# Kernel optimization log

Measured on AMD Instinct MI355X. Metric: run time of the kernel, lower is better.

The kernel has to match this reference:

```python
import jax, jax.numpy as jnp
import numpy as np

NUM_HEADS = 2
LN_EPS = 1e-5
NEG_MASK = -1e9


def setup_inputs() -> dict:
    key = jax.random.key(0)
    ks = jax.random.split(key, 8)
    B, C, T, N = 8, 64, 32, 400
    H, D = NUM_HEADS, C // NUM_HEADS
    s = 1.0 / np.sqrt(C)
    return {
        "x": jax.random.normal(ks[0], (B, C, T, N), dtype=jnp.float32),
        "Wq": jax.random.normal(ks[1], (C, C), dtype=jnp.float32) * s,
        "Wk": jax.random.normal(ks[2], (C, C), dtype=jnp.float32) * s,
        "Wv": jax.random.normal(ks[3], (C, C), dtype=jnp.float32) * s,
        "a_src": jax.random.normal(ks[4], (H, D), dtype=jnp.float32) * 0.1,
        "a_dst": jax.random.normal(ks[5], (H, D), dtype=jnp.float32) * 0.1,
        "ln_gamma": jnp.ones((C,), dtype=jnp.float32),
        "ln_beta": jnp.zeros((C,), dtype=jnp.float32),
        "gso": jax.random.randint(ks[6], (N, N), 0, 2, dtype=jnp.int32),
    }


def reference(x, Wq, Wk, Wv, a_src, a_dst, ln_gamma, ln_beta, gso):
    B, C, T, N = x.shape
    H = NUM_HEADS
    D = C // H
    # (B,C,T,N) -> (B*T, N, C)
    xr = jnp.transpose(x, (0, 2, 3, 1)).reshape(B * T, N, C)
    # torch Linear: y = x @ W.T; then split heads -> (BT, N, H, D)
    Q = (xr @ Wq.T).reshape(B * T, N, H, D)
    K = (xr @ Wk.T).reshape(B * T, N, H, D)
    V = (xr @ Wv.T).reshape(B * T, N, H, D)
    # GAT additive scores per head
    s_src = jnp.einsum("bnhd,hd->bnh", Q, a_src)  # (BT, N, H)
    s_dst = jnp.einsum("bnhd,hd->bnh", K, a_dst)  # (BT, N, H)
    scores = s_src[:, :, None, :] + s_dst[:, None, :, :]  # (BT, i, j, H)
    scores = jax.nn.leaky_relu(scores, negative_slope=0.2)
    mask = jnp.where(gso == 0, jnp.float32(NEG_MASK), 0.0)  # (N, N)
    scores = scores + mask[None, :, :, None]
    attn = jax.nn.softmax(scores, axis=2)  # softmax over dst j; dropout = identity (eval)
    out = jnp.einsum("bijh,bjhd->bihd", attn, V).reshape(B * T, N, C)
    # LayerNorm over channel dim
    mu = jnp.mean(out, axis=-1, keepdims=True)
    var = jnp.var(out, axis=-1, keepdims=True)
    out = (out - mu) * jax.lax.rsqrt(var + LN_EPS) * ln_gamma + ln_beta
    # (BT, N, C) -> (B, C, T, N)
    return jnp.transpose(out.reshape(B, T, N, C), (0, 3, 1, 2))
```

## Files before the change

### kernel.cpp

```cpp
#include <hip/hip_runtime.h>
#include <hip/hip_bf16.h>

typedef __attribute__((ext_vector_type(8))) short bf16x8;
typedef __attribute__((ext_vector_type(4))) float f32x4;
typedef __attribute__((ext_vector_type(4))) int i32x4;
typedef __attribute__((ext_vector_type(4))) unsigned int u32x4;

#define B_   8
#define C_   64
#define T_   32
#define N_   400
#define BT_  256
#define NKT_ 13
#define CN_  12800
#define VROW 424
#define WROW 72
#define L2E_ 1.4426950408889634f
#define C2_  (-13.849872392533959f)
#define SH12_ (-17.312340490667560f)

#if __has_builtin(__builtin_amdgcn_exp2f)
#define EXP2F(x) __builtin_amdgcn_exp2f(x)
#else
#define EXP2F(x) __expf((x) * 0.6931471805599453f)
#endif

__global__ __launch_bounds__(256) void gat_prep(
    const int* __restrict__ gso, unsigned int* __restrict__ mb)
{
  int idx = blockIdx.x*256 + threadIdx.x;
  if (idx < N_*16) {
    int i = idx >> 4, kw = idx & 15;
    unsigned int bits = 0;
    if (kw < 13) {
      int j0 = kw * 32;
      #pragma unroll
      for (int bb = 0; bb < 32; ++bb) {
        int j = j0 + bb;
        if (j < N_ && gso[i*N_ + j] != 0) bits |= (1u << bb);
      }
    }
    mb[idx] = bits;
  }
}

__global__ __launch_bounds__(1024) void gat_fused(
    const float* __restrict__ x, const float* __restrict__ Wq,
    const float* __restrict__ Wk, const float* __restrict__ Wv,
    const float* __restrict__ a_src, const float* __restrict__ a_dst,
    const float* __restrict__ gamma, const float* __restrict__ beta,
    const unsigned int* __restrict__ mb, float* __restrict__ out)
{
  __shared__ __align__(16) __hip_bfloat16 Vt[64][VROW];
  __shared__ __align__(16) __hip_bfloat16 wvb[80][WROW];
  __shared__ __align__(16) float sd_s[2][416];
  __shared__ __align__(16) float si_s[2][400];
  __shared__ __align__(16) float ob[128][68];
  __shared__ float g_s[64], b_s[64];

  const int tid = threadIdx.x;
  const int bt = blockIdx.x;
  const int b = bt >> 5, t = bt & 31;
  const int lane = tid & 63, wave = tid >> 6;
  const int col = lane & 15, quad = lane >> 4;

  #pragma unroll
  for (int it = 0; it < 4; ++it) {
    int idx = it*1024 + tid;
    int o = idx >> 6, c = idx & 63;
    wvb[o][c] = __float2bfloat16(Wv[o*C_ + c]);
  }
  if (tid < 256) {
    int ww = tid >> 6, c = tid & 63, h = ww >> 1;
    const float* W = (ww & 1) ? Wk : Wq;
    const float* a = (ww & 1) ? a_dst : a_src;
    float s = 0.f;
    #pragma unroll
    for (int d = 0; d < 32; ++d) s += W[(h*32 + d)*C_ + c] * a[h*32 + d];
    wvb[64 + ww][c] = __float2bfloat16(s * L2E_);
  } else if (tid < 320) {
    g_s[tid - 256] = gamma[tid - 256];
  } else if (tid < 384) {
    b_s[tid - 320] = beta[tid - 320];
  } else if (tid < 416) {
    int tt = tid - 384;
    sd_s[tt >> 4][400 + (tt & 15)] = 0.f;
  }
  for (int idx = tid; idx < 12*WROW; idx += 1024)
    wvb[68 + idx/WROW][idx % WROW] = __float2bfloat16(0.f);
  for (int idx = tid; idx < 64*24; idx += 1024)
    Vt[idx/24][400 + idx%24] = __float2bfloat16(0.f);
  __syncthreads();

  {
    const float* xbase = x + ((size_t)b*C_*T_ + t)*N_;
    for (int nt = wave; nt < 25; nt += 16) {
      const int n0 = nt*16;
      bf16x8 bfrag[2];
      #pragma unroll
      for (int kt = 0; kt < 2; ++kt) {
        const float* xc = xbase + (size_t)(kt*32 + quad*8)*CN_ + n0 + col;
        union { short s[8]; bf16x8 v; } pk;
        #pragma unroll
        for (int j = 0; j < 8; ++j) {
          union { __hip_bfloat16 h; short s; } cv;
          cv.h = __float2bfloat16(xc[(size_t)j*CN_]);
          pk.s[j] = cv.s;
        }
        bfrag[kt] = pk.v;
      }
      #pragma unroll
      for (int ot = 0; ot < 5; ++ot) {
        f32x4 acc = {0.f, 0.f, 0.f, 0.f};
        #pragma unroll
        for (int kt = 0; kt < 2; ++kt) {
          bf16x8 afr = *(const bf16x8*)&wvb[ot*16 + col][kt*32 + quad*8];
          acc = __builtin_amdgcn_mfma_f32_16x16x32_bf16(afr, bfrag[kt], acc, 0, 0, 0);
        }
        if (ot < 4) {
          #pragma unroll
          for (int r = 0; r < 4; ++r)
            Vt[ot*16 + quad*4 + r][n0 + col] = __float2bfloat16(acc[r]);
        } else if (quad == 0) {
          #pragma unroll
          for (int r = 0; r < 4; ++r) {
            int h = r >> 1;
            if (r & 1) sd_s[h][n0 + col] = acc[r];
            else       si_s[h][n0 + col] = acc[r] + SH12_;
          }
        }
      }
    }
  }
  __syncthreads();

  const int hh = wave & 1, itile = wave >> 1;
  const int rowA = col;

  bf16x8 ones;
  #pragma unroll
  for (int k = 0; k < 8; ++k) ones[k] = (short)0x3F80;

  for (int r0 = 0; r0 < N_; r0 += 128) {
    const int ibase = r0 + itile*16;
    if (ibase < N_) {
      const int irow = ibase + rowA;
      const float si1 = si_s[hh][irow];
      const u32x4* mp = (const u32x4*)(mb + irow*16);
      u32x4 mw0 = mp[0], mw1 = mp[1], mw2 = mp[2];
      unsigned int mw12 = mb[irow*16 + 12];
      const float* sdp = sd_s[hh] + quad*8;
      const __hip_bfloat16* v0p = &Vt[hh*32 + rowA][quad*8];
      const __hip_bfloat16* v1p = v0p + 16*VROW;

      f32x4 d0 = {0,0,0,0}, d1 = {0,0,0,0}, d2 = {0,0,0,0};
      #pragma unroll
      for (int kt = 0; kt < NKT_; ++kt) {
        unsigned int mword = (kt < 4) ? mw0[kt] : (kt < 8) ? mw1[kt-4]
                           : (kt < 12) ? mw2[kt-8] : mw12;
        unsigned int mbyte = (mword >> (quad*8)) & 0xffu;
        f32x4 s0 = *(const f32x4*)(sdp + kt*32);
        f32x4 s1 = *(const f32x4*)(sdp + kt*32 + 4);
        bf16x8 vb0 = *(const bf16x8*)(v0p + kt*32);
        bf16x8 vb1 = *(const bf16x8*)(v1p + kt*32);
        int em[8];
        #pragma unroll
        for (int jj = 0; jj < 8; ++jj) {
          float sd = (jj < 4) ? s0[jj] : s1[jj-4];
          float t1 = si1 + sd;
          float t2 = fmaf(0.2f, t1, C2_);
          float v  = fmaxf(t1, t2);
          float e  = EXP2F(v);
          int msk = ((int)(mbyte << (31 - jj))) >> 31;
          em[jj] = __float_as_int(e) & msk;
        }
        union { i32x4 i; bf16x8 v; } af;
        af.i.x = (int)__builtin_amdgcn_perm((unsigned)em[1], (unsigned)em[0], 0x07060302u);
        af.i.y = (int)__builtin_amdgcn_perm((unsigned)em[3], (unsigned)em[2], 0x07060302u);
        af.i.z = (int)__builtin_amdgcn_perm((unsigned)em[5], (unsigned)em[4], 0x07060302u);
        af.i.w = (int)__builtin_amdgcn_perm((unsigned)em[7], (unsigned)em[6], 0x07060302u);
        d0 = __builtin_amdgcn_mfma_f32_16x16x32_bf16(af.v, vb0, d0, 0, 0, 0);
        d1 = __builtin_amdgcn_mfma_f32_16x16x32_bf16(af.v, vb1, d1, 0, 0, 0);
        d2 = __builtin_amdgcn_mfma_f32_16x16x32_bf16(af.v, ones, d2, 0, 0, 0);
      }
      #pragma unroll
      for (int r = 0; r < 4; ++r) {
        float li = 1.0f / d2[r];
        int rl = itile*16 + quad*4 + r;
        ob[rl][hh*32 + rowA]      = d0[r] * li;
        ob[rl][hh*32 + 16 + rowA] = d1[r] * li;
      }
    }
    __syncthreads();

    {
      int rl = tid >> 3, cgi = tid & 7;
      int n = r0 + rl;
      if (n < N_) {
        float u[8]; float s = 0.f;
        #pragma unroll
        for (int k = 0; k < 8; ++k) { u[k] = ob[rl][cgi*8 + k]; s += u[k]; }
        s += __shfl_xor(s,1); s += __shfl_xor(s,2); s += __shfl_xor(s,4);
        float mu = s * (1.f/64.f);
        float q = 0.f;
        #pragma unroll
        for (int k = 0; k < 8; ++k) { float dv = u[k]-mu; q = fmaf(dv,dv,q); }
        q += __shfl_xor(q,1); q += __shfl_xor(q,2); q += __shfl_xor(q,4);
        float rstd = rsqrtf(q*(1.f/64.f) + 1e-5f);
        #pragma unroll
        for (int k = 0; k < 8; ++k)
          ob[rl][cgi*8 + k] = (u[k]-mu)*rstd*g_s[cgi*8 + k] + b_s[cgi*8 + k];
      }
    }
    __syncthreads();

    #pragma unroll
    for (int it = 0; it < 8; ++it) {
      int idx = it*1024 + tid;
      int c = idx >> 7, nn = idx & 127;
      int n = r0 + nn;
      if (n < N_) out[((size_t)(b*C_ + c)*T_ + t)*N_ + n] = ob[nn][c];
    }
    __syncthreads();
  }
}

extern "C" void kernel_launch(void* const* d_in, const int* in_sizes, int n_in,
                              void* d_out, int out_size, void* d_ws, size_t ws_size,
                              hipStream_t stream) {
  (void)in_sizes; (void)n_in; (void)out_size; (void)ws_size;
  const float* x     = (const float*)d_in[0];
  const float* Wq    = (const float*)d_in[1];
  const float* Wk    = (const float*)d_in[2];
  const float* Wv    = (const float*)d_in[3];
  const float* a_src = (const float*)d_in[4];
  const float* a_dst = (const float*)d_in[5];
  const float* gamma = (const float*)d_in[6];
  const float* beta  = (const float*)d_in[7];
  const int*   gso   = (const int*)d_in[8];
  float* out = (float*)d_out;

  unsigned int* mb = (unsigned int*)d_ws;

  gat_prep<<<26, 256, 0, stream>>>(gso, mb);
  gat_fused<<<BT_, 1024, 0, stream>>>(x, Wq, Wk, Wv, a_src, a_dst,
                                      gamma, beta, mb, out);
}
```

Before: 122.4 us.

## Split each batch-time slice across two 512-thread blocks with aliased LDS

Launches two 512-thread blocks per (b,t) slice, each handling half of the query rows, so there are 512 blocks instead of 256 with smaller per-block LDS. The wvb and ob buffers are aliased into one scratch array to cut shared memory. x loads for the projection are software-prefetched into registers one tile ahead. The cost is that each block recomputes the full V/score projection, doubling that work and the x reads.

```diff
diff --git a/kernel.cpp b/kernel.cpp
--- a/kernel.cpp
+++ b/kernel.cpp
@@ -15,6 +15,7 @@
 #define CN_  12800
 #define VROW 424
 #define WROW 72
+#define OBW  65
 #define L2E_ 1.4426950408889634f
 #define C2_  (-13.849872392533959f)
 #define SH12_ (-17.312340490667560f)
@@ -44,7 +45,7 @@
   }
 }
 
-__global__ __launch_bounds__(1024) void gat_fused(
+__global__ __launch_bounds__(512, 4) void gat_fused(
     const float* __restrict__ x, const float* __restrict__ Wq,
     const float* __restrict__ Wk, const float* __restrict__ Wv,
     const float* __restrict__ a_src, const float* __restrict__ a_dst,
@@ -52,21 +53,38 @@
     const unsigned int* __restrict__ mb, float* __restrict__ out)
 {
   __shared__ __align__(16) __hip_bfloat16 Vt[64][VROW];
-  __shared__ __align__(16) __hip_bfloat16 wvb[80][WROW];
+  __shared__ __align__(16) char scr[16640];
   __shared__ __align__(16) float sd_s[2][416];
   __shared__ __align__(16) float si_s[2][400];
-  __shared__ __align__(16) float ob[128][68];
   __shared__ float g_s[64], b_s[64];
 
+  __hip_bfloat16 (*wvb)[WROW] = (__hip_bfloat16(*)[WROW])scr;
+  float (*ob)[OBW] = (float(*)[OBW])scr;
+
   const int tid = threadIdx.x;
-  const int bt = blockIdx.x;
+  const int bt = blockIdx.x >> 1, half = blockIdx.x & 1;
   const int b = bt >> 5, t = bt & 31;
   const int lane = tid & 63, wave = tid >> 6;
   const int col = lane & 15, quad = lane >> 4;
+  const int i_start = half ? 208 : 0;
+  const int i_end   = half ? 400 : 208;
+
+  const float* xbase = x + ((size_t)b*C_*T_ + t)*N_;
+
+  float xf[16];
+  {
+    const int n0 = wave*16;
+    const float* xc0 = xbase + (size_t)(quad*8)*CN_ + n0 + col;
+    const float* xc1 = xbase + (size_t)(32 + quad*8)*CN_ + n0 + col;
+    #pragma unroll
+    for (int j = 0; j < 8; ++j) xf[j]     = xc0[(size_t)j*CN_];
+    #pragma unroll
+    for (int j = 0; j < 8; ++j) xf[8 + j] = xc1[(size_t)j*CN_];
+  }
 
   #pragma unroll
-  for (int it = 0; it < 4; ++it) {
-    int idx = it*1024 + tid;
+  for (int it = 0; it < 8; ++it) {
+    int idx = it*512 + tid;
     int o = idx >> 6, c = idx & 63;
     wvb[o][c] = __float2bfloat16(Wv[o*C_ + c]);
   }
@@ -86,48 +104,53 @@
     int tt = tid - 384;
     sd_s[tt >> 4][400 + (tt & 15)] = 0.f;
   }
-  for (int idx = tid; idx < 12*WROW; idx += 1024)
+  for (int idx = tid; idx < 12*WROW; idx += 512)
     wvb[68 + idx/WROW][idx % WROW] = __float2bfloat16(0.f);
-  for (int idx = tid; idx < 64*24; idx += 1024)
+  for (int idx = tid; idx < 64*24; idx += 512)
     Vt[idx/24][400 + idx%24] = __float2bfloat16(0.f);
   __syncthreads();
 
-  {
-    const float* xbase = x + ((size_t)b*C_*T_ + t)*N_;
-    for (int nt = wave; nt < 25; nt += 16) {
-      const int n0 = nt*16;
-      bf16x8 bfrag[2];
+  for (int nt = wave; nt < 25; nt += 8) {
+    const int n0 = nt*16;
+    bf16x8 bfrag[2];
+    #pragma unroll
+    for (int kt = 0; kt < 2; ++kt) {
+      union { short s[8]; bf16x8 v; } pk;
+      #pragma unroll
+      for (int j = 0; j < 8; ++j) {
+        union { __hip_bfloat16 h; short s; } cv;
+        cv.h = __float2bfloat16(xf[kt*8 + j]);
+        pk.s[j] = cv.s;
+      }
+      bfrag[kt] = pk.v;
+    }
+    const int ntn = nt + 8;
+    if (ntn < 25) {
+      const float* xc0 = xbase + (size_t)(quad*8)*CN_ + ntn*16 + col;
+      const float* xc1 = xbase + (size_t)(32 + quad*8)*CN_ + ntn*16 + col;
+      #pragma unroll
+      for (int j = 0; j < 8; ++j) xf[j]     = xc0[(size_t)j*CN_];
+      #pragma unroll
+      for (int j = 0; j < 8; ++j) xf[8 + j] = xc1[(size_t)j*CN_];
+    }
+    #pragma unroll
+    for (int ot = 0; ot < 5; ++ot) {
+      f32x4 acc = {0.f, 0.f, 0.f, 0.f};
       #pragma unroll
       for (int kt = 0; kt < 2; ++kt) {
-        const float* xc = xbase + (size_t)(kt*32 + quad*8)*CN_ + n0 + col;
-        union { short s[8]; bf16x8 v; } pk;
-        #pragma unroll
-        for (int j = 0; j < 8; ++j) {
-          union { __hip_bfloat16 h; short s; } cv;
-          cv.h = __float2bfloat16(xc[(size_t)j*CN_]);
-          pk.s[j] = cv.s;
-        }
-        bfrag[kt] = pk.v;
-      }
-      #pragma unroll
-      for (int ot = 0; ot < 5; ++ot) {
-        f32x4 acc = {0.f, 0.f, 0.f, 0.f};
-        #pragma unroll
-        for (int kt = 0; kt < 2; ++kt) {
-          bf16x8 afr = *(const bf16x8*)&wvb[ot*16 + col][kt*32 + quad*8];
-          acc = __builtin_amdgcn_mfma_f32_16x16x32_bf16(afr, bfrag[kt], acc, 0, 0, 0);
-        }
-        if (ot < 4) {
-          #pragma unroll
-          for (int r = 0; r < 4; ++r)
-            Vt[ot*16 + quad*4 + r][n0 + col] = __float2bfloat16(acc[r]);
-        } else if (quad == 0) {
-          #pragma unroll
-          for (int r = 0; r < 4; ++r) {
-            int h = r >> 1;
-            if (r & 1) sd_s[h][n0 + col] = acc[r];
-            else       si_s[h][n0 + col] = acc[r] + SH12_;
-          }
+        bf16x8 afr = *(const bf16x8*)&wvb[ot*16 + col][kt*32 + quad*8];
+        acc = __builtin_amdgcn_mfma_f32_16x16x32_bf16(afr, bfrag[kt], acc, 0, 0, 0);
+      }
+      if (ot < 4) {
+        #pragma unroll
+        for (int r = 0; r < 4; ++r)
+          Vt[ot*16 + quad*4 + r][n0 + col] = __float2bfloat16(acc[r]);
+      } else if (quad == 0) {
+        #pragma unroll
+        for (int r = 0; r < 4; ++r) {
+          int h = r >> 1;
+          if (r & 1) sd_s[h][n0 + col] = acc[r];
+          else       si_s[h][n0 + col] = acc[r] + SH12_;
         }
       }
     }
@@ -141,9 +164,9 @@
   #pragma unroll
   for (int k = 0; k < 8; ++k) ones[k] = (short)0x3F80;
 
-  for (int r0 = 0; r0 < N_; r0 += 128) {
+  for (int r0 = i_start; r0 < i_end; r0 += 64) {
     const int ibase = r0 + itile*16;
-    if (ibase < N_) {
+    if (ibase < i_end) {
       const int irow = ibase + rowA;
       const float si1 = si_s[hh][irow];
       const u32x4* mp = (const u32x4*)(mb + irow*16);
@@ -196,7 +219,7 @@
     {
       int rl = tid >> 3, cgi = tid & 7;
       int n = r0 + rl;
-      if (n < N_) {
+      if (n < i_end) {
         float u[8]; float s = 0.f;
         #pragma unroll
         for (int k = 0; k < 8; ++k) { u[k] = ob[rl][cgi*8 + k]; s += u[k]; }
@@ -216,10 +239,10 @@
 
     #pragma unroll
     for (int it = 0; it < 8; ++it) {
-      int idx = it*1024 + tid;
-      int c = idx >> 7, nn = idx & 127;
+      int idx = it*512 + tid;
+      int c = idx >> 6, nn = idx & 63;
       int n = r0 + nn;
-      if (n < N_) out[((size_t)(b*C_ + c)*T_ + t)*N_ + n] = ob[nn][c];
+      if (n < i_end) out[((size_t)(b*C_ + c)*T_ + t)*N_ + n] = ob[nn][c];
     }
     __syncthreads();
   }
@@ -243,6 +266,6 @@
   unsigned int* mb = (unsigned int*)d_ws;
 
   gat_prep<<<26, 256, 0, stream>>>(gso, mb);
-  gat_fused<<<BT_, 1024, 0, stream>>>(x, Wq, Wk, Wv, a_src, a_dst,
-                                      gamma, beta, mb, out);
+  gat_fused<<<BT_*2, 512, 0, stream>>>(x, Wq, Wk, Wv, a_src, a_dst,
+                                       gamma, beta, mb, out);
 }
```

New measurement: 126.7 us. +3.5%, slower.

## Fuse LayerNorm into attention waves and store output directly from registers

Applied to the files above, without the earlier changes.

Each wave now handles one 16-row tile for both heads and runs LayerNorm in registers using cross-lane shuffles. It then writes float4 vectors straight to global memory, which removes the shared ob buffer, the per-128-row passes and their three barriers. The x loads are issued before the weight setup so their latency overlaps it, the projection weight fragments are hoisted into registers, and the reciprocal uses the hardware rcp builtin. In exchange, waves are imbalanced (25 tiles over 16 waves), register pressure is higher, and rcp gives slightly lower precision.

```diff
diff --git a/kernel.cpp b/kernel.cpp
--- a/kernel.cpp
+++ b/kernel.cpp
@@ -24,6 +24,11 @@
 #else
 #define EXP2F(x) __expf((x) * 0.6931471805599453f)
 #endif
+#if __has_builtin(__builtin_amdgcn_rcpf)
+#define RCPF(x) __builtin_amdgcn_rcpf(x)
+#else
+#define RCPF(x) (1.0f / (x))
+#endif
 
 __global__ __launch_bounds__(256) void gat_prep(
     const int* __restrict__ gso, unsigned int* __restrict__ mb)
@@ -55,7 +60,6 @@
   __shared__ __align__(16) __hip_bfloat16 wvb[80][WROW];
   __shared__ __align__(16) float sd_s[2][416];
   __shared__ __align__(16) float si_s[2][400];
-  __shared__ __align__(16) float ob[128][68];
   __shared__ float g_s[64], b_s[64];
 
   const int tid = threadIdx.x;
@@ -63,6 +67,19 @@
   const int b = bt >> 5, t = bt & 31;
   const int lane = tid & 63, wave = tid >> 6;
   const int col = lane & 15, quad = lane >> 4;
+
+  const float* xbase = x + ((size_t)b*C_*T_ + t)*N_;
+
+  float xf[16];
+  {
+    const int n0 = wave*16;
+    const float* xc0 = xbase + (size_t)(quad*8)*CN_ + n0 + col;
+    const float* xc1 = xbase + (size_t)(32 + quad*8)*CN_ + n0 + col;
+    #pragma unroll
+    for (int j = 0; j < 8; ++j) xf[j]     = xc0[(size_t)j*CN_];
+    #pragma unroll
+    for (int j = 0; j < 8; ++j) xf[8 + j] = xc1[(size_t)j*CN_];
+  }
 
   #pragma unroll
   for (int it = 0; it < 4; ++it) {
@@ -86,47 +103,65 @@
     int tt = tid - 384;
     sd_s[tt >> 4][400 + (tt & 15)] = 0.f;
   }
-  for (int idx = tid; idx < 12*WROW; idx += 1024)
-    wvb[68 + idx/WROW][idx % WROW] = __float2bfloat16(0.f);
+  if (tid < 12*WROW)
+    wvb[68 + tid/WROW][tid % WROW] = __float2bfloat16(0.f);
   for (int idx = tid; idx < 64*24; idx += 1024)
     Vt[idx/24][400 + idx%24] = __float2bfloat16(0.f);
   __syncthreads();
 
   {
-    const float* xbase = x + ((size_t)b*C_*T_ + t)*N_;
-    for (int nt = wave; nt < 25; nt += 16) {
-      const int n0 = nt*16;
-      bf16x8 bfrag[2];
-      #pragma unroll
-      for (int kt = 0; kt < 2; ++kt) {
-        const float* xc = xbase + (size_t)(kt*32 + quad*8)*CN_ + n0 + col;
-        union { short s[8]; bf16x8 v; } pk;
-        #pragma unroll
-        for (int j = 0; j < 8; ++j) {
-          union { __hip_bfloat16 h; short s; } cv;
-          cv.h = __float2bfloat16(xc[(size_t)j*CN_]);
-          pk.s[j] = cv.s;
-        }
-        bfrag[kt] = pk.v;
-      }
-      #pragma unroll
-      for (int ot = 0; ot < 5; ++ot) {
-        f32x4 acc = {0.f, 0.f, 0.f, 0.f};
+    bf16x8 afr[5][2];
+    #pragma unroll
+    for (int ot = 0; ot < 5; ++ot)
+      #pragma unroll
+      for (int kt = 0; kt < 2; ++kt)
+        afr[ot][kt] = *(const bf16x8*)&wvb[ot*16 + col][kt*32 + quad*8];
+
+    const int nt2 = wave + 16;
+    float xg[16];
+    if (nt2 < 25) {
+      const float* xc0 = xbase + (size_t)(quad*8)*CN_ + nt2*16 + col;
+      const float* xc1 = xbase + (size_t)(32 + quad*8)*CN_ + nt2*16 + col;
+      #pragma unroll
+      for (int j = 0; j < 8; ++j) xg[j]     = xc0[(size_t)j*CN_];
+      #pragma unroll
+      for (int j = 0; j < 8; ++j) xg[8 + j] = xc1[(size_t)j*CN_];
+    }
+
+    #pragma unroll
+    for (int task = 0; task < 2; ++task) {
+      const int nt = (task == 0) ? wave : nt2;
+      if (nt < 25) {
+        const int n0 = nt*16;
+        const float* src = (task == 0) ? xf : xg;
+        bf16x8 bfrag[2];
         #pragma unroll
         for (int kt = 0; kt < 2; ++kt) {
-          bf16x8 afr = *(const bf16x8*)&wvb[ot*16 + col][kt*32 + quad*8];
-          acc = __builtin_amdgcn_mfma_f32_16x16x32_bf16(afr, bfrag[kt], acc, 0, 0, 0);
+          union { short s[8]; bf16x8 v; } pk;
+          #pragma unroll
+          for (int j = 0; j < 8; ++j) {
+            union { __hip_bfloat16 h; short s; } cv;
+            cv.h = __float2bfloat16(src[kt*8 + j]);
+            pk.s[j] = cv.s;
+          }
+          bfrag[kt] = pk.v;
         }
-        if (ot < 4) {
-          #pragma unroll
-          for (int r = 0; r < 4; ++r)
-            Vt[ot*16 + quad*4 + r][n0 + col] = __float2bfloat16(acc[r]);
-        } else if (quad == 0) {
-          #pragma unroll
-          for (int r = 0; r < 4; ++r) {
-            int h = r >> 1;
-            if (r & 1) sd_s[h][n0 + col] = acc[r];
-            else       si_s[h][n0 + col] = acc[r] + SH12_;
+        #pragma unroll
+        for (int ot = 0; ot < 5; ++ot) {
+          f32x4 acc = {0.f, 0.f, 0.f, 0.f};
+          acc = __builtin_amdgcn_mfma_f32_16x16x32_bf16(afr[ot][0], bfrag[0], acc, 0, 0, 0);
+          acc = __builtin_amdgcn_mfma_f32_16x16x32_bf16(afr[ot][1], bfrag[1], acc, 0, 0, 0);
+          if (ot < 4) {
+            #pragma unroll
+            for (int r = 0; r < 4; ++r)
+              Vt[ot*16 + quad*4 + r][n0 + col] = __float2bfloat16(acc[r]);
+          } else if (quad == 0) {
+            #pragma unroll
+            for (int r = 0; r < 4; ++r) {
+              int h = r >> 1;
+              if (r & 1) sd_s[h][n0 + col] = acc[r];
+              else       si_s[h][n0 + col] = acc[r] + SH12_;
+            }
           }
         }
       }
@@ -134,26 +169,29 @@
   }
   __syncthreads();
 
-  const int hh = wave & 1, itile = wave >> 1;
-  const int rowA = col;
-
-  bf16x8 ones;
+  float gg[4], bb[4];
   #pragma unroll
-  for (int k = 0; k < 8; ++k) ones[k] = (short)0x3F80;
-
-  for (int r0 = 0; r0 < N_; r0 += 128) {
-    const int ibase = r0 + itile*16;
-    if (ibase < N_) {
-      const int irow = ibase + rowA;
+  for (int k = 0; k < 4; ++k) { gg[k] = g_s[16*k + col]; bb[k] = b_s[16*k + col]; }
+
+  for (int tl = wave; tl < 25; tl += 16) {
+    const int ibase = tl*16;
+    const int irow = ibase + col;
+    const u32x4* mp = (const u32x4*)(mb + irow*16);
+    u32x4 mw0 = mp[0], mw1 = mp[1], mw2 = mp[2];
+    unsigned int mw12 = mb[irow*16 + 12];
+
+    float u[4][4];
+    #pragma unroll
+    for (int hh = 0; hh < 2; ++hh) {
       const float si1 = si_s[hh][irow];
-      const u32x4* mp = (const u32x4*)(mb + irow*16);
-      u32x4 mw0 = mp[0], mw1 = mp[1], mw2 = mp[2];
-      unsigned int mw12 = mb[irow*16 + 12];
       const float* sdp = sd_s[hh] + quad*8;
-      const __hip_bfloat16* v0p = &Vt[hh*32 + rowA][quad*8];
+      const __hip_bfloat16* v0p = &Vt[hh*32 + col][quad*8];
       const __hip_bfloat16* v1p = v0p + 16*VROW;
-
       f32x4 d0 = {0,0,0,0}, d1 = {0,0,0,0}, d2 = {0,0,0,0};
+      bf16x8 ones;
+      #pragma unroll
+      for (int k = 0; k < 8; ++k) ones[k] = (short)0x3F80;
+
       #pragma unroll
       for (int kt = 0; kt < NKT_; ++kt) {
         unsigned int mword = (kt < 4) ? mw0[kt] : (kt < 8) ? mw1[kt-4]
@@ -185,43 +223,33 @@
       }
       #pragma unroll
       for (int r = 0; r < 4; ++r) {
-        float li = 1.0f / d2[r];
-        int rl = itile*16 + quad*4 + r;
-        ob[rl][hh*32 + rowA]      = d0[r] * li;
-        ob[rl][hh*32 + 16 + rowA] = d1[r] * li;
-      }
-    }
-    __syncthreads();
-
-    {
-      int rl = tid >> 3, cgi = tid & 7;
-      int n = r0 + rl;
-      if (n < N_) {
-        float u[8]; float s = 0.f;
-        #pragma unroll
-        for (int k = 0; k < 8; ++k) { u[k] = ob[rl][cgi*8 + k]; s += u[k]; }
-        s += __shfl_xor(s,1); s += __shfl_xor(s,2); s += __shfl_xor(s,4);
-        float mu = s * (1.f/64.f);
-        float q = 0.f;
-        #pragma unroll
-        for (int k = 0; k < 8; ++k) { float dv = u[k]-mu; q = fmaf(dv,dv,q); }
-        q += __shfl_xor(q,1); q += __shfl_xor(q,2); q += __shfl_xor(q,4);
-        float rstd = rsqrtf(q*(1.f/64.f) + 1e-5f);
-        #pragma unroll
-        for (int k = 0; k < 8; ++k)
-          ob[rl][cgi*8 + k] = (u[k]-mu)*rstd*g_s[cgi*8 + k] + b_s[cgi*8 + k];
-      }
-    }
-    __syncthreads();
-
-    #pragma unroll
-    for (int it = 0; it < 8; ++it) {
-      int idx = it*1024 + tid;
-      int c = idx >> 7, nn = idx & 127;
-      int n = r0 + nn;
-      if (n < N_) out[((size_t)(b*C_ + c)*T_ + t)*N_ + n] = ob[nn][c];
-    }
-    __syncthreads();
+        float li = RCPF(d2[r]);
+        u[2*hh + 0][r] = d0[r] * li;
+        u[2*hh + 1][r] = d1[r] * li;
+      }
+    }
+
+    f32x4 o[4];
+    #pragma unroll
+    for (int r = 0; r < 4; ++r) {
+      float s = u[0][r] + u[1][r] + u[2][r] + u[3][r];
+      s += __shfl_xor(s,1); s += __shfl_xor(s,2);
+      s += __shfl_xor(s,4); s += __shfl_xor(s,8);
+      float mu = s * (1.f/64.f);
+      float q = 0.f;
+      #pragma unroll
+      for (int k = 0; k < 4; ++k) { float dv = u[k][r]-mu; q = fmaf(dv,dv,q); }
+      q += __shfl_xor(q,1); q += __shfl_xor(q,2);
+      q += __shfl_xor(q,4); q += __shfl_xor(q,8);
+      float rstd = rsqrtf(q*(1.f/64.f) + 1e-5f);
+      #pragma unroll
+      for (int k = 0; k < 4; ++k)
+        o[k][r] = (u[k][r]-mu)*rstd*gg[k] + bb[k];
+    }
+    float* obase = out + (((size_t)b*C_ + col)*T_ + t)*N_ + ibase + quad*4;
+    #pragma unroll
+    for (int k = 0; k < 4; ++k)
+      *(f32x4*)(obase + (size_t)16*k*T_*N_) = o[k];
   }
 }
 
```

Measured after the change: 344.7 us. 182% more time.
